# Kernel tuning notes

Measured on AMD Instinct MI355X. Metric: run time of the kernel, lower is better.

## Reference

```python
import jax, jax.numpy as jnp
import numpy as np

N_MODEL = 1024
N_HEADS = 16
KV_HEADS = 4
HEAD_DIM = N_MODEL // N_HEADS          # 64
KV_MODEL = HEAD_DIM * KV_HEADS         # 256
GROUPS = N_HEADS // KV_HEADS           # 4
B, S = 4, 2048


def _rmsnorm(x):
    return x * jax.lax.rsqrt(jnp.mean(x * x, axis=-1, keepdims=True) + 1e-6)


def _act_quant(x):
    # 8-bit absmax per-token quantization (BitNet b1.58)
    scale = 127.0 / jnp.clip(jnp.max(jnp.abs(x), axis=-1, keepdims=True), 1e-5)
    return jnp.clip(jnp.round(x * scale), -128.0, 127.0) / scale


def _weight_quant(w):
    # ternary absmean quantization
    scale = 1.0 / jnp.clip(jnp.mean(jnp.abs(w)), 1e-5)
    return jnp.clip(jnp.round(w * scale), -1.0, 1.0) / scale


def bitlinear(x, w, b):
    xn = _rmsnorm(x)
    xq = xn + jax.lax.stop_gradient(_act_quant(xn) - xn)   # STE
    wq = w + jax.lax.stop_gradient(_weight_quant(w) - w)   # STE
    return jnp.einsum('...i,oi->...o', xq, wq) + b


def setup_inputs() -> dict:
    key = jax.random.key(0)
    ks = jax.random.split(key, 11)
    sq = 1.0 / np.sqrt(N_MODEL)
    sk = 1.0 / np.sqrt(KV_MODEL)
    return {
        'query': jax.random.normal(ks[0], (B, S, N_MODEL), jnp.float32),
        'key':   jax.random.normal(ks[1], (B, S, N_MODEL), jnp.float32),
        'value': jax.random.normal(ks[2], (B, S, N_MODEL), jnp.float32),
        'Wq': jax.random.normal(ks[3], (N_MODEL, N_MODEL), jnp.float32) * sq,
        'bq': jnp.zeros((N_MODEL,), jnp.float32),
        'Wk': jax.random.normal(ks[4], (KV_MODEL, N_MODEL), jnp.float32) * sq,
        'bk': jnp.zeros((KV_MODEL,), jnp.float32),
        'Wv': jax.random.normal(ks[5], (KV_MODEL, N_MODEL), jnp.float32) * sq,
        'bv': jnp.zeros((KV_MODEL,), jnp.float32),
        'Wo': jax.random.normal(ks[6], (N_MODEL, KV_MODEL), jnp.float32) * sk,
        'bo': jnp.zeros((N_MODEL,), jnp.float32),
    }


def reference(query, key, value, Wq, bq, Wk, bk, Wv, bv, Wo, bo):
    b = query.shape[0]
    Q = bitlinear(query, Wq, bq)   # [b, n, n_model]
    K = bitlinear(key,   Wk, bk)   # [b, s, kv_model]
    V = bitlinear(value, Wv, bv)   # [b, s, kv_model]

    # [b, h, n, d] layouts
    Q = Q.reshape(b, -1, N_HEADS, HEAD_DIM).transpose(0, 2, 1, 3)
    K = K.reshape(b, -1, KV_HEADS, HEAD_DIM).transpose(0, 2, 1, 3)
    V = V.reshape(b, -1, KV_HEADS, HEAD_DIM).transpose(0, 2, 1, 3)

    # group query heads: [b, g, kv_h, n, d]
    Qg = Q.reshape(b, KV_HEADS, GROUPS, -1, HEAD_DIM).transpose(0, 2, 1, 3, 4)
    # NOTE: faithful to the module, the einsum output has no 'g' axis,
    # so the grouped query heads are SUMMED over g.
    energy = jnp.einsum('bghnd,bhsd->bhns', Qg, K)  # [b, kv_h, n, s]

    scale = jnp.sqrt(jnp.float32(HEAD_DIM))
    attention = jax.nn.softmax(energy / scale, axis=-1)
    x = jnp.einsum('bhns,bhsd->bhnd', attention, V)  # [b, kv_h, n, d]
    x = x.transpose(0, 2, 1, 3).reshape(b, -1, KV_MODEL)
    x = bitlinear(x, Wo, bo)       # [b, n, n_model]
    return (x, attention)
```

## Files before the change

### kernel.cpp

```cpp
#include <hip/hip_runtime.h>
#include <stdint.h>

#define N_MODELC 1024
#define KV_MODELC 256
#define BATCH 4
#define SEQ 2048
#define NTOK (BATCH*SEQ)

typedef __attribute__((ext_vector_type(4))) float f32x4;
typedef __attribute__((ext_vector_type(4))) int   i32x4;
typedef __attribute__((ext_vector_type(8))) short s16x8;

__device__ __forceinline__ unsigned short f2bf(float f){
  unsigned u = __builtin_bit_cast(unsigned, f);
  u = (u + 0x7FFFu + ((u>>16)&1u)) >> 16;
  return (unsigned short)u;
}

__global__ __launch_bounds__(256) void k_actquant1024(
    const float* __restrict__ xq_in, const float* __restrict__ xk_in, const float* __restrict__ xv_in,
    int8_t* __restrict__ q8q, int8_t* __restrict__ q8k, int8_t* __restrict__ q8v,
    float* __restrict__ scq, float* __restrict__ sck, float* __restrict__ scv)
{
  int row = blockIdx.x, which = blockIdx.y, t = threadIdx.x;
  const float* x = (which==0)?xq_in:(which==1)?xk_in:xv_in;
  int8_t* q8 = (which==0)?q8q:(which==1)?q8k:q8v;
  float* sc = (which==0)?scq:(which==1)?sck:scv;
  const float* xr = x + (size_t)row*N_MODELC;
  float4 v = reinterpret_cast<const float4*>(xr)[t];
  float ss = v.x*v.x + v.y*v.y + v.z*v.z + v.w*v.w;
  float am = fmaxf(fmaxf(fabsf(v.x),fabsf(v.y)), fmaxf(fabsf(v.z),fabsf(v.w)));
  #pragma unroll
  for (int m=32;m;m>>=1){ ss += __shfl_xor(ss,m,64); am = fmaxf(am, __shfl_xor(am,m,64)); }
  __shared__ float red[8];
  int wid = t>>6;
  if ((t&63)==0){ red[wid]=ss; red[4+wid]=am; }
  __syncthreads();
  ss = red[0]+red[1]+red[2]+red[3];
  am = fmaxf(fmaxf(red[4],red[5]), fmaxf(red[6],red[7]));
  float rinv = rsqrtf(ss*(1.0f/N_MODELC) + 1e-6f);
  float clipv = fmaxf(am*rinv, 1e-5f);
  float qs = 127.0f/clipv;
  float fsc = rinv*qs;
  char4 o;
  o.x = (signed char)(int)fminf(127.f, fmaxf(-128.f, rintf(v.x*fsc)));
  o.y = (signed char)(int)fminf(127.f, fmaxf(-128.f, rintf(v.y*fsc)));
  o.z = (signed char)(int)fminf(127.f, fmaxf(-128.f, rintf(v.z*fsc)));
  o.w = (signed char)(int)fminf(127.f, fmaxf(-128.f, rintf(v.w*fsc)));
  reinterpret_cast<char4*>(q8 + (size_t)row*N_MODELC)[t] = o;
  if (t==0) sc[row] = clipv*(1.0f/127.0f);
}

__global__ __launch_bounds__(64) void k_actquant256(
    const float* __restrict__ X, int8_t* __restrict__ q8, float* __restrict__ sc)
{
  int row = blockIdx.x, l = threadIdx.x;
  float4 v = reinterpret_cast<const float4*>(X + (size_t)row*KV_MODELC)[l];
  float ss = v.x*v.x + v.y*v.y + v.z*v.z + v.w*v.w;
  float am = fmaxf(fmaxf(fabsf(v.x),fabsf(v.y)), fmaxf(fabsf(v.z),fabsf(v.w)));
  #pragma unroll
  for (int m=32;m;m>>=1){ ss += __shfl_xor(ss,m,64); am = fmaxf(am, __shfl_xor(am,m,64)); }
  float rinv = rsqrtf(ss*(1.0f/KV_MODELC) + 1e-6f);
  float clipv = fmaxf(am*rinv, 1e-5f);
  float qs = 127.0f/clipv;
  float fsc = rinv*qs;
  char4 o;
  o.x = (signed char)(int)fminf(127.f, fmaxf(-128.f, rintf(v.x*fsc)));
  o.y = (signed char)(int)fminf(127.f, fmaxf(-128.f, rintf(v.y*fsc)));
  o.z = (signed char)(int)fminf(127.f, fmaxf(-128.f, rintf(v.z*fsc)));
  o.w = (signed char)(int)fminf(127.f, fmaxf(-128.f, rintf(v.w*fsc)));
  reinterpret_cast<char4*>(q8 + (size_t)row*KV_MODELC)[l] = o;
  if (l==0) sc[row] = clipv*(1.0f/127.0f);
}

__global__ __launch_bounds__(256) void k_wabs_partial(
    const float* __restrict__ Wq, const float* __restrict__ Wk,
    const float* __restrict__ Wv, const float* __restrict__ Wo, float* __restrict__ partial)
{
  int mat = blockIdx.y;
  const float* w = (mat==0)?Wq:(mat==1)?Wk:(mat==2)?Wv:Wo;
  int n = (mat==0)?(N_MODELC*N_MODELC):(KV_MODELC*N_MODELC);
  float s = 0.f;
  for (int i = blockIdx.x*256 + threadIdx.x; i < n; i += 256*256) s += fabsf(w[i]);
  #pragma unroll
  for (int m=32;m;m>>=1) s += __shfl_xor(s,m,64);
  __shared__ float red[4];
  int wid = threadIdx.x>>6;
  if ((threadIdx.x&63)==0) red[wid]=s;
  __syncthreads();
  if (threadIdx.x==0) partial[mat*256 + blockIdx.x] = red[0]+red[1]+red[2]+red[3];
}

__global__ __launch_bounds__(256) void k_wfinal(const float* __restrict__ partial, float* __restrict__ wfac)
{
  int mat = blockIdx.x, t = threadIdx.x;
  float s = partial[mat*256 + t];
  #pragma unroll
  for (int m=32;m;m>>=1) s += __shfl_xor(s,m,64);
  __shared__ float red[4];
  int wid = t>>6;
  if ((t&63)==0) red[wid]=s;
  __syncthreads();
  if (t==0){
    float tot = red[0]+red[1]+red[2]+red[3];
    float n = (mat==0)?(float)(N_MODELC*N_MODELC):(float)(KV_MODELC*N_MODELC);
    wfac[mat] = fmaxf(tot/n, 1e-5f);
  }
}

__global__ __launch_bounds__(256) void k_tern(
    const float* __restrict__ Wq, const float* __restrict__ Wk,
    const float* __restrict__ Wv, const float* __restrict__ Wo,
    const float* __restrict__ wfac,
    int8_t* __restrict__ Wqs, int8_t* __restrict__ Wkt,
    int8_t* __restrict__ Wvt, int8_t* __restrict__ Wot)
{
  int mat = blockIdx.y;
  int idx = blockIdx.x*256 + threadIdx.x;
  if (mat==0){
    float s = 1.0f/wfac[0];
    int op = idx>>10, i = idx&1023;
    int kv = op>>6, d = op&63;
    int acc = 0;
    #pragma unroll
    for (int g=0; g<4; g++){
      float w = Wq[(size_t)(kv*256 + g*64 + d)*N_MODELC + i];
      float r = fminf(1.f, fmaxf(-1.f, rintf(w*s)));
      acc += (int)r;
    }
    Wqs[idx] = (int8_t)acc;
  } else {
    const float* w = (mat==1)?Wk:(mat==2)?Wv:Wo;
    int8_t* o = (mat==1)?Wkt:(mat==2)?Wvt:Wot;
    float s = 1.0f/wfac[mat];
    float r = fminf(1.f, fmaxf(-1.f, rintf(w[idx]*s)));
    o[idx] = (int8_t)r;
  }
}

template<int KDIM, int MODE>
__global__ __launch_bounds__(256) void k_gemm_i8(
    const int8_t* __restrict__ A, const int8_t* __restrict__ B,
    const float* __restrict__ rowscale, const float* __restrict__ wfac, int wfi,
    const float* __restrict__ bias, void* __restrict__ outp)
{
  int mb = blockIdx.x*64, nb = blockIdx.y*64;
  int w = threadIdx.x>>6, l = threadIdx.x&63, lr = l&15, lk = l>>4;
  const int8_t* Ap = A + (size_t)(mb + w*16 + lr)*KDIM + lk*16;
  const int8_t* Bp = B + (size_t)(nb + lr)*KDIM + lk*16;
  i32x4 acc[4];
  #pragma unroll
  for (int f=0; f<4; f++) acc[f] = i32x4{0,0,0,0};
  #pragma unroll 4
  for (int kk=0; kk<KDIM; kk+=64){
    i32x4 a = *reinterpret_cast<const i32x4*>(Ap + kk);
    #pragma unroll
    for (int f=0; f<4; f++){
      i32x4 b = *reinterpret_cast<const i32x4*>(Bp + (size_t)f*16*KDIM + kk);
      acc[f] = __builtin_amdgcn_mfma_i32_16x16x64_i8(a, b, acc[f], 0, 0, 0);
    }
  }
  float wf = wfac[wfi];
  #pragma unroll
  for (int f=0; f<4; f++){
    int col = nb + f*16 + lr;
    float bval;
    if constexpr (MODE==0){
      int kv = col>>6, d = col&63;
      const float* bb = bias + kv*256 + d;
      bval = bb[0]+bb[64]+bb[128]+bb[192];
    } else {
      bval = bias[col];
    }
    #pragma unroll
    for (int r=0; r<4; r++){
      int row = mb + w*16 + lk*4 + r;
      float val = (float)acc[f][r] * (rowscale[row]*wf) + bval;
      if constexpr (MODE==0){
        ((unsigned short*)outp)[(size_t)row*KV_MODELC + col] = f2bf(0.125f*val);
      } else if constexpr (MODE==1){
        ((unsigned short*)outp)[(size_t)row*KV_MODELC + col] = f2bf(val);
      } else if constexpr (MODE==2){
        int bi = row>>11, s = row&2047;
        ((unsigned short*)outp)[((size_t)(bi*256 + col))*SEQ + s] = f2bf(val);
      } else {
        ((float*)outp)[(size_t)row*N_MODELC + col] = val;
      }
    }
  }
}

__global__ __launch_bounds__(256) void k_attn(
    const unsigned short* __restrict__ Qs, const unsigned short* __restrict__ Kb,
    float* __restrict__ attn)
{
  int bkv = blockIdx.y, b = bkv>>2, kv = bkv&3;
  int rt = blockIdx.x;
  int w = threadIdx.x>>6, l = threadIdx.x&63, lr = l&15, lk = l>>4;
  int rowt = rt*64 + w*16;
  size_t tq = (size_t)(b*SEQ + rowt + lr)*KV_MODELC + kv*64 + lk*8;
  s16x8 qa0 = *reinterpret_cast<const s16x8*>(Qs + tq);
  s16x8 qa1 = *reinterpret_cast<const s16x8*>(Qs + tq + 32);
  const unsigned short* kbase = Kb + (size_t)b*SEQ*KV_MODELC + kv*64 + lk*8;
  float m[4], ll[4];
  #pragma unroll
  for (int r=0;r<4;r++){ m[r] = -INFINITY; ll[r] = 0.f; }
  for (int st=0; st<SEQ; st+=16){
    const unsigned short* kp = kbase + (size_t)(st+lr)*KV_MODELC;
    s16x8 k0 = *reinterpret_cast<const s16x8*>(kp);
    s16x8 k1 = *reinterpret_cast<const s16x8*>(kp + 32);
    f32x4 acc = {0.f,0.f,0.f,0.f};
    acc = __builtin_amdgcn_mfma_f32_16x16x32_bf16(qa0, k0, acc, 0,0,0);
    acc = __builtin_amdgcn_mfma_f32_16x16x32_bf16(qa1, k1, acc, 0,0,0);
    #pragma unroll
    for (int r=0;r<4;r++){
      float e = acc[r];
      float mn = fmaxf(m[r], e);
      ll[r] = ll[r]*__expf(m[r]-mn) + __expf(e-mn);
      m[r] = mn;
    }
  }
  #pragma unroll
  for (int r=0;r<4;r++){
    #pragma unroll
    for (int mask=1; mask<16; mask<<=1){
      float om = __shfl_xor(m[r], mask, 64);
      float ol = __shfl_xor(ll[r], mask, 64);
      float mn = fmaxf(m[r], om);
      ll[r] = ll[r]*__expf(m[r]-mn) + ol*__expf(om-mn);
      m[r] = mn;
    }
  }
  float invl[4];
  #pragma unroll
  for (int r=0;r<4;r++) invl[r] = 1.0f/ll[r];
  float* arow = attn + (size_t)bkv*SEQ*SEQ;
  for (int st=0; st<SEQ; st+=16){
    const unsigned short* kp = kbase + (size_t)(st+lr)*KV_MODELC;
    s16x8 k0 = *reinterpret_cast<const s16x8*>(kp);
    s16x8 k1 = *reinterpret_cast<const s16x8*>(kp + 32);
    f32x4 acc = {0.f,0.f,0.f,0.f};
    acc = __builtin_amdgcn_mfma_f32_16x16x32_bf16(qa0, k0, acc, 0,0,0);
    acc = __builtin_amdgcn_mfma_f32_16x16x32_bf16(qa1, k1, acc, 0,0,0);
    #pragma unroll
    for (int r=0;r<4;r++){
      float p = __expf(acc[r]-m[r])*invl[r];
      arow[(size_t)(rowt + lk*4 + r)*SEQ + st + lr] = p;
    }
  }
}

__global__ __launch_bounds__(256) void k_pv(
    const float* __restrict__ attn, const unsigned short* __restrict__ VT,
    float* __restrict__ X)
{
  int bkv = blockIdx.y, b = bkv>>2, kv = bkv&3;
  int nt = blockIdx.x;
  int w = threadIdx.x>>6, l = threadIdx.x&63, lr = l&15, lk = l>>4;
  int rowt = nt*64 + w*16;
  const float* arow = attn + (size_t)(bkv*SEQ + rowt + lr)*SEQ + lk*8;
  const unsigned short* vbase = VT + ((size_t)(b*256 + kv*64))*SEQ + lk*8;
  f32x4 acc[4];
  #pragma unroll
  for (int dt=0; dt<4; dt++) acc[dt] = f32x4{0.f,0.f,0.f,0.f};
  for (int sc=0; sc<SEQ; sc+=32){
    float4 a0 = *reinterpret_cast<const float4*>(arow + sc);
    float4 a1 = *reinterpret_cast<const float4*>(arow + sc + 4);
    s16x8 af;
    af[0]=(short)f2bf(a0.x); af[1]=(short)f2bf(a0.y);
    af[2]=(short)f2bf(a0.z); af[3]=(short)f2bf(a0.w);
    af[4]=(short)f2bf(a1.x); af[5]=(short)f2bf(a1.y);
    af[6]=(short)f2bf(a1.z); af[7]=(short)f2bf(a1.w);
    #pragma unroll
    for (int dt=0; dt<4; dt++){
      s16x8 bf = *reinterpret_cast<const s16x8*>(vbase + (size_t)(dt*16+lr)*SEQ + sc);
      acc[dt] = __builtin_amdgcn_mfma_f32_16x16x32_bf16(af, bf, acc[dt], 0,0,0);
    }
  }
  int token = b*SEQ + rowt + lk*4;
  #pragma unroll
  for (int dt=0; dt<4; dt++){
    #pragma unroll
    for (int r=0; r<4; r++){
      X[(size_t)(token + r)*KV_MODELC + kv*64 + dt*16 + lr] = acc[dt][r];
    }
  }
}

extern "C" void kernel_launch(void* const* d_in, const int* in_sizes, int n_in,
                              void* d_out, int out_size, void* d_ws, size_t ws_size,
                              hipStream_t stream)
{
  (void)in_sizes; (void)n_in; (void)out_size; (void)ws_size;
  const float* q  = (const float*)d_in[0];
  const float* k  = (const float*)d_in[1];
  const float* v  = (const float*)d_in[2];
  const float* Wq = (const float*)d_in[3];
  const float* bq = (const float*)d_in[4];
  const float* Wk = (const float*)d_in[5];
  const float* bk = (const float*)d_in[6];
  const float* Wv = (const float*)d_in[7];
  const float* bv = (const float*)d_in[8];
  const float* Wo = (const float*)d_in[9];
  const float* bo = (const float*)d_in[10];

  float* out_x = (float*)d_out;
  float* out_attn = out_x + (size_t)NTOK*N_MODELC;

  char* ws = (char*)d_ws;
  size_t off = 0;
  auto alloc = [&](size_t bytes)->void*{
    void* p = ws + off; off += (bytes + 255) & ~(size_t)255; return p;
  };
  int8_t* q8q = (int8_t*)alloc((size_t)NTOK*N_MODELC);
  int8_t* q8k = (int8_t*)alloc((size_t)NTOK*N_MODELC);
  int8_t* q8v = (int8_t*)alloc((size_t)NTOK*N_MODELC);
  int8_t* q8x = (int8_t*)alloc((size_t)NTOK*KV_MODELC);
  float* scq = (float*)alloc(NTOK*4);
  float* sck = (float*)alloc(NTOK*4);
  float* scv = (float*)alloc(NTOK*4);
  float* scx = (float*)alloc(NTOK*4);
  float* partial = (float*)alloc(4*256*4);
  float* wfac = (float*)alloc(256);
  int8_t* Wqs = (int8_t*)alloc(256*1024);
  int8_t* Wkt = (int8_t*)alloc(256*1024);
  int8_t* Wvt = (int8_t*)alloc(256*1024);
  int8_t* Wot = (int8_t*)alloc(1024*256);
  unsigned short* Qs = (unsigned short*)alloc((size_t)NTOK*KV_MODELC*2);
  unsigned short* Kb = (unsigned short*)alloc((size_t)NTOK*KV_MODELC*2);
  unsigned short* VT = (unsigned short*)alloc((size_t)NTOK*KV_MODELC*2);
  float* X = (float*)alloc((size_t)NTOK*KV_MODELC*4);

  hipLaunchKernelGGL(k_actquant1024, dim3(NTOK,3), dim3(256), 0, stream,
                     q,k,v, q8q,q8k,q8v, scq,sck,scv);
  hipLaunchKernelGGL(k_wabs_partial, dim3(256,4), dim3(256), 0, stream, Wq,Wk,Wv,Wo, partial);
  hipLaunchKernelGGL(k_wfinal, dim3(4), dim3(256), 0, stream, partial, wfac);
  hipLaunchKernelGGL(k_tern, dim3(1024,4), dim3(256), 0, stream,
                     Wq,Wk,Wv,Wo, wfac, Wqs,Wkt,Wvt,Wot);
  hipLaunchKernelGGL((k_gemm_i8<1024,0>), dim3(128,4), dim3(256), 0, stream,
                     q8q, Wqs, scq, wfac, 0, bq, (void*)Qs);
  hipLaunchKernelGGL((k_gemm_i8<1024,1>), dim3(128,4), dim3(256), 0, stream,
                     q8k, Wkt, sck, wfac, 1, bk, (void*)Kb);
  hipLaunchKernelGGL((k_gemm_i8<1024,2>), dim3(128,4), dim3(256), 0, stream,
                     q8v, Wvt, scv, wfac, 2, bv, (void*)VT);
  hipLaunchKernelGGL(k_attn, dim3(32,16), dim3(256), 0, stream, Qs, Kb, out_attn);
  hipLaunchKernelGGL(k_pv, dim3(32,16), dim3(256), 0, stream, out_attn, VT, X);
  hipLaunchKernelGGL(k_actquant256, dim3(NTOK), dim3(64), 0, stream, X, q8x, scx);
  hipLaunchKernelGGL((k_gemm_i8<256,3>), dim3(128,16), dim3(256), 0, stream,
                     q8x, Wot, scx, wfac, 3, bo, (void*)out_x);
}
```

Before: 375.7 us.

## Fuse softmax-probability write with PV matmul to avoid re-reading attention

```diff
diff --git a/kernel.cpp b/kernel.cpp
--- a/kernel.cpp
+++ b/kernel.cpp
@@ -190,18 +190,22 @@
   }
 }
 
-__global__ __launch_bounds__(256) void k_attn(
+__global__ __launch_bounds__(256) void k_attn_pv(
     const unsigned short* __restrict__ Qs, const unsigned short* __restrict__ Kb,
-    float* __restrict__ attn)
-{
+    const unsigned short* __restrict__ VT,
+    float* __restrict__ attn, float* __restrict__ X)
+{
+  __shared__ unsigned short plds[64][64];
   int bkv = blockIdx.y, b = bkv>>2, kv = bkv&3;
-  int rt = blockIdx.x;
   int w = threadIdx.x>>6, l = threadIdx.x&63, lr = l&15, lk = l>>4;
-  int rowt = rt*64 + w*16;
+  int brow = blockIdx.x*64;
+  int rowt = brow + w*16;
   size_t tq = (size_t)(b*SEQ + rowt + lr)*KV_MODELC + kv*64 + lk*8;
   s16x8 qa0 = *reinterpret_cast<const s16x8*>(Qs + tq);
   s16x8 qa1 = *reinterpret_cast<const s16x8*>(Qs + tq + 32);
   const unsigned short* kbase = Kb + (size_t)b*SEQ*KV_MODELC + kv*64 + lk*8;
+  const unsigned short* vbase = VT + ((size_t)(b*256 + kv*64))*SEQ;
+
   float m[4], ll[4];
   #pragma unroll
   for (int r=0;r<4;r++){ m[r] = -INFINITY; ll[r] = 0.f; }
@@ -234,47 +238,43 @@
   float invl[4];
   #pragma unroll
   for (int r=0;r<4;r++) invl[r] = 1.0f/ll[r];
-  float* arow = attn + (size_t)bkv*SEQ*SEQ;
-  for (int st=0; st<SEQ; st+=16){
-    const unsigned short* kp = kbase + (size_t)(st+lr)*KV_MODELC;
-    s16x8 k0 = *reinterpret_cast<const s16x8*>(kp);
-    s16x8 k1 = *reinterpret_cast<const s16x8*>(kp + 32);
-    f32x4 acc = {0.f,0.f,0.f,0.f};
-    acc = __builtin_amdgcn_mfma_f32_16x16x32_bf16(qa0, k0, acc, 0,0,0);
-    acc = __builtin_amdgcn_mfma_f32_16x16x32_bf16(qa1, k1, acc, 0,0,0);
-    #pragma unroll
-    for (int r=0;r<4;r++){
-      float p = __expf(acc[r]-m[r])*invl[r];
-      arow[(size_t)(rowt + lk*4 + r)*SEQ + st + lr] = p;
-    }
-  }
-}
-
-__global__ __launch_bounds__(256) void k_pv(
-    const float* __restrict__ attn, const unsigned short* __restrict__ VT,
-    float* __restrict__ X)
-{
-  int bkv = blockIdx.y, b = bkv>>2, kv = bkv&3;
-  int nt = blockIdx.x;
-  int w = threadIdx.x>>6, l = threadIdx.x&63, lr = l&15, lk = l>>4;
-  int rowt = nt*64 + w*16;
-  const float* arow = attn + (size_t)(bkv*SEQ + rowt + lr)*SEQ + lk*8;
-  const unsigned short* vbase = VT + ((size_t)(b*256 + kv*64))*SEQ + lk*8;
-  f32x4 acc[4];
-  #pragma unroll
-  for (int dt=0; dt<4; dt++) acc[dt] = f32x4{0.f,0.f,0.f,0.f};
-  for (int sc=0; sc<SEQ; sc+=32){
-    float4 a0 = *reinterpret_cast<const float4*>(arow + sc);
-    float4 a1 = *reinterpret_cast<const float4*>(arow + sc + 4);
-    s16x8 af;
-    af[0]=(short)f2bf(a0.x); af[1]=(short)f2bf(a0.y);
-    af[2]=(short)f2bf(a0.z); af[3]=(short)f2bf(a0.w);
-    af[4]=(short)f2bf(a1.x); af[5]=(short)f2bf(a1.y);
-    af[6]=(short)f2bf(a1.z); af[7]=(short)f2bf(a1.w);
+
+  float* arow = attn + (size_t)bkv*SEQ*SEQ + (size_t)brow*SEQ;
+  f32x4 acco[4];
+  #pragma unroll
+  for (int dt=0; dt<4; dt++) acco[dt] = f32x4{0.f,0.f,0.f,0.f};
+  int qw = w*16 + lk*4;
+  int qr = w*16 + lr;
+  int rsw = (qr&7)<<3;
+
+  for (int st=0; st<SEQ; st+=64){
+    #pragma unroll
+    for (int sub=0; sub<4; sub++){
+      int s0 = st + sub*16;
+      const unsigned short* kp = kbase + (size_t)(s0+lr)*KV_MODELC;
+      s16x8 k0 = *reinterpret_cast<const s16x8*>(kp);
+      s16x8 k1 = *reinterpret_cast<const s16x8*>(kp + 32);
+      f32x4 acc = {0.f,0.f,0.f,0.f};
+      acc = __builtin_amdgcn_mfma_f32_16x16x32_bf16(qa0, k0, acc, 0,0,0);
+      acc = __builtin_amdgcn_mfma_f32_16x16x32_bf16(qa1, k1, acc, 0,0,0);
+      int slocal = sub*16 + lr;
+      #pragma unroll
+      for (int r=0;r<4;r++){
+        float p = __expf(acc[r]-m[r])*invl[r];
+        arow[(size_t)(qw + r)*SEQ + s0 + lr] = p;
+        int sw = (slocal & 7) | ((((slocal>>3) ^ ((qw+r)&7)))<<3);
+        plds[qw + r][sw] = f2bf(p);
+      }
+    }
+    s16x8 a0 = *reinterpret_cast<const s16x8*>(&plds[qr][lk<<3 ^ rsw]);
+    s16x8 a1 = *reinterpret_cast<const s16x8*>(&plds[qr][(4+lk)<<3 ^ rsw]);
     #pragma unroll
     for (int dt=0; dt<4; dt++){
-      s16x8 bf = *reinterpret_cast<const s16x8*>(vbase + (size_t)(dt*16+lr)*SEQ + sc);
-      acc[dt] = __builtin_amdgcn_mfma_f32_16x16x32_bf16(af, bf, acc[dt], 0,0,0);
+      const unsigned short* vp = vbase + (size_t)(dt*16+lr)*SEQ + st + lk*8;
+      s16x8 b0 = *reinterpret_cast<const s16x8*>(vp);
+      s16x8 b1 = *reinterpret_cast<const s16x8*>(vp + 32);
+      acco[dt] = __builtin_amdgcn_mfma_f32_16x16x32_bf16(a0, b0, acco[dt], 0,0,0);
+      acco[dt] = __builtin_amdgcn_mfma_f32_16x16x32_bf16(a1, b1, acco[dt], 0,0,0);
     }
   }
   int token = b*SEQ + rowt + lk*4;
@@ -282,7 +282,7 @@
   for (int dt=0; dt<4; dt++){
     #pragma unroll
     for (int r=0; r<4; r++){
-      X[(size_t)(token + r)*KV_MODELC + kv*64 + dt*16 + lr] = acc[dt][r];
+      X[(size_t)(token + r)*KV_MODELC + kv*64 + dt*16 + lr] = acco[dt][r];
     }
   }
 }
@@ -343,8 +343,8 @@
                      q8k, Wkt, sck, wfac, 1, bk, (void*)Kb);
   hipLaunchKernelGGL((k_gemm_i8<1024,2>), dim3(128,4), dim3(256), 0, stream,
                      q8v, Wvt, scv, wfac, 2, bv, (void*)VT);
-  hipLaunchKernelGGL(k_attn, dim3(32,16), dim3(256), 0, stream, Qs, Kb, out_attn);
-  hipLaunchKernelGGL(k_pv, dim3(32,16), dim3(256), 0, stream, out_attn, VT, X);
+  hipLaunchKernelGGL(k_attn_pv, dim3(32,16), dim3(256), 0, stream,
+                     Qs, Kb, VT, out_attn, X);
   hipLaunchKernelGGL(k_actquant256, dim3(NTOK), dim3(64), 0, stream, X, q8x, scx);
   hipLaunchKernelGGL((k_gemm_i8<256,3>), dim3(128,16), dim3(256), 0, stream,
                      q8x, Wot, scx, wfac, 3, bo, (void*)out_x);
```

Measured after the change: 342.5 us. 8.8% less time.
